# Performance work log

Measured on AMD Instinct MI355X. Metric: run time of the kernel, lower is better.

Reference implementation:

```python
import jax, jax.numpy as jnp
import numpy as np

N = 10000          # nodes
E = 80000          # edges
STATE_DIM = 18
HID = 1024
LAYERS = 4


def setup_inputs() -> dict:
    key = jax.random.key(0)
    ks = jax.random.split(key, 16)
    s = 0.02
    x = jax.random.normal(ks[0], (N, STATE_DIM), dtype=jnp.float32)
    edge_index = jax.random.randint(ks[1], (2, E), 0, N, dtype=jnp.int32)
    # frozen inverse-phase embedding projection (no bias)
    proj_w = jax.random.normal(ks[2], (STATE_DIM, HID), dtype=jnp.float32) * s
    # per-layer message MLP: Linear(2*HID -> HID) -> ReLU -> Linear(HID -> HID)
    W1 = jax.random.normal(ks[3], (LAYERS, 2 * HID, HID), dtype=jnp.float32) * s
    b1 = jnp.zeros((LAYERS, HID), dtype=jnp.float32)
    W2 = jax.random.normal(ks[4], (LAYERS, HID, HID), dtype=jnp.float32) * s
    b2 = jnp.zeros((LAYERS, HID), dtype=jnp.float32)
    # ghost head: Linear(HID->256) -> ReLU -> Linear(256->1) -> Sigmoid
    gw1 = jax.random.normal(ks[5], (HID, 256), dtype=jnp.float32) * s
    gb1 = jnp.zeros((256,), dtype=jnp.float32)
    gw2 = jax.random.normal(ks[6], (256, 1), dtype=jnp.float32) * s
    gb2 = jnp.zeros((1,), dtype=jnp.float32)
    # state head: Linear(HID -> STATE_DIM)
    sw = jax.random.normal(ks[7], (HID, STATE_DIM), dtype=jnp.float32) * s
    sb = jnp.zeros((STATE_DIM,), dtype=jnp.float32)
    return {"x": x, "edge_index": edge_index, "proj_w": proj_w,
            "W1": W1, "b1": b1, "W2": W2, "b2": b2,
            "gw1": gw1, "gb1": gb1, "gw2": gw2, "gb2": gb2,
            "sw": sw, "sb": sb}


def reference(x, edge_index, proj_w, W1, b1, W2, b2, gw1, gb1, gw2, gb2, sw, sb):
    src = edge_index[0]  # j (source)
    dst = edge_index[1]  # i (target), aggr='add' scatters into i
    # InversePhaseEmbedding: sin(h)*cos(h)
    p = x @ proj_w                      # [N, HID]
    h = jnp.sin(p) * jnp.cos(p)
    for l in range(LAYERS):
        x_i = h[dst]                    # [E, HID] gather target feats
        x_j = h[src]                    # [E, HID] gather source feats
        msg = jnp.concatenate([x_i, x_j - x_i], axis=-1)  # [E, 2*HID]
        m = jax.nn.relu(msg @ W1[l] + b1[l]) @ W2[l] + b2[l]  # [E, HID]
        h = jax.ops.segment_sum(m, dst, num_segments=N)       # scatter-add
        h = jax.nn.relu(h)
    ghost_score = jax.nn.sigmoid(jax.nn.relu(h @ gw1 + gb1) @ gw2 + gb2)  # [N,1]
    stable_state = h @ sw + sb                                            # [N,18]
    return ghost_score, stable_state, h
```

## Files before the change

kernel.cpp:

```cpp
#include <hip/hip_runtime.h>
#include <hip/hip_bf16.h>
#include <math.h>

#define NN 10000
#define EE 80000
#define SDIM 18
#define HID 1024
#define NLAYERS 4
#define GHID 256

typedef __bf16 bf16;
typedef __bf16 bf16x8 __attribute__((ext_vector_type(8)));
typedef __bf16 bf16x4 __attribute__((ext_vector_type(4)));
typedef float f32x4 __attribute__((ext_vector_type(4)));

#define AS1C(p) ((const __attribute__((address_space(1))) void*)(p))
#define AS3(p)  ((__attribute__((address_space(3))) void*)(p))

__global__ void count_kernel(const int* __restrict__ ei, int* __restrict__ cnt) {
    int e = blockIdx.x * 256 + threadIdx.x;
    if (e < EE) atomicAdd(&cnt[ei[EE + e]], 1);
}

__global__ __launch_bounds__(256) void scan_kernel(const int* __restrict__ cnt,
                                                   int* __restrict__ offs,
                                                   int* __restrict__ cursor,
                                                   float* __restrict__ degF) {
    const int CH = 40;
    __shared__ int partial[256];
    int t = threadIdx.x;
    int base = t * CH;
    int local[CH];
    int sum = 0;
#pragma unroll
    for (int i = 0; i < CH; ++i) {
        int idx = base + i;
        int v = (idx < NN) ? cnt[idx] : 0;
        local[i] = sum;
        sum += v;
    }
    partial[t] = sum;
    __syncthreads();
    for (int off = 1; off < 256; off <<= 1) {
        int v = (t >= off) ? partial[t - off] : 0;
        __syncthreads();
        partial[t] += v;
        __syncthreads();
    }
    int excl = (t == 0) ? 0 : partial[t - 1];
#pragma unroll
    for (int i = 0; i < CH; ++i) {
        int idx = base + i;
        if (idx < NN) {
            int o = excl + local[i];
            offs[idx] = o;
            cursor[idx] = o;
            degF[idx] = (float)cnt[idx];
        }
    }
    if (t == 255) offs[NN] = partial[255];
}

__global__ void scatter_kernel(const int* __restrict__ ei, int* __restrict__ cursor,
                               int* __restrict__ esrc) {
    int e = blockIdx.x * 256 + threadIdx.x;
    if (e < EE) {
        int dst = ei[EE + e];
        int pos = atomicAdd(&cursor[dst], 1);
        esrc[pos] = ei[e];
    }
}

__global__ __launch_bounds__(256) void prep_kernel(const float* __restrict__ W1,
                                                   const float* __restrict__ W2,
                                                   const float* __restrict__ gw1,
                                                   const float* __restrict__ sw,
                                                   const float* __restrict__ b1,
                                                   bf16* __restrict__ WT,
                                                   bf16* __restrict__ W2t,
                                                   bf16* __restrict__ gw1t,
                                                   bf16* __restrict__ swt,
                                                   float* __restrict__ cb,
                                                   int* __restrict__ cnt) {
    __shared__ float td[32][33];
    __shared__ float tb[32][33];
    const size_t H2 = (size_t)HID * HID;
    int b = blockIdx.x;
    int tx = threadIdx.x & 31, ty = threadIdx.x >> 5;

    if (b < 4096) {
        int l = b >> 10, r = b & 1023;
        int bx = (r & 31) * 32, by = (r >> 5) * 32;
        const float* s = W1 + (size_t)l * 2 * H2;
        bf16* d = WT + (size_t)l * 2 * H2;
#pragma unroll
        for (int r4 = 0; r4 < 4; ++r4) {
            int row = by + ty + r4 * 8;
            float vt = s[(size_t)row * HID + bx + tx];
            float vb = s[H2 + (size_t)row * HID + bx + tx];
            td[ty + r4 * 8][tx] = vt - vb;
            tb[ty + r4 * 8][tx] = vb;
        }
        __syncthreads();
#pragma unroll
        for (int r4 = 0; r4 < 4; ++r4) {
            int orow = bx + ty + r4 * 8;
            d[(size_t)orow * HID + by + tx] = (bf16)td[tx][ty + r4 * 8];
            d[(size_t)(HID + orow) * HID + by + tx] = (bf16)tb[tx][ty + r4 * 8];
        }
    } else if (b < 8192) {
        int sub = b - 4096;
        int l = sub >> 10, r = sub & 1023;
        int bx = (r & 31) * 32, by = (r >> 5) * 32;
        const float* s = W2 + (size_t)l * H2;
        bf16* d = W2t + (size_t)l * H2;
#pragma unroll
        for (int r4 = 0; r4 < 4; ++r4) {
            int row = by + ty + r4 * 8;
            td[ty + r4 * 8][tx] = s[(size_t)row * HID + bx + tx];
        }
        __syncthreads();
#pragma unroll
        for (int r4 = 0; r4 < 4; ++r4) {
            int orow = bx + ty + r4 * 8;
            d[(size_t)orow * HID + by + tx] = (bf16)td[tx][ty + r4 * 8];
        }
    } else if (b < 8448) {
        int sub = b - 8192;
        int bx = (sub & 7) * 32, by = (sub >> 3) * 32;
#pragma unroll
        for (int r4 = 0; r4 < 4; ++r4) {
            int row = by + ty + r4 * 8;
            td[ty + r4 * 8][tx] = gw1[(size_t)row * GHID + bx + tx];
        }
        __syncthreads();
#pragma unroll
        for (int r4 = 0; r4 < 4; ++r4) {
            int orow = bx + ty + r4 * 8;
            gw1t[(size_t)orow * HID + by + tx] = (bf16)td[tx][ty + r4 * 8];
        }
    } else if (b < 8576) {
        int i = (b - 8448) * 256 + threadIdx.x;
        int n = i >> 10, k = i & 1023;
        swt[i] = (bf16)(n < SDIM ? sw[k * SDIM + n] : 0.f);
    } else if (b < 8608) {
        int i = (b - 8576) * 256 + threadIdx.x;
        int l = i >> 11, c = i & 2047;
        cb[i] = (c < HID) ? b1[l * HID + c] : 0.f;
    } else {
        int i = (b - 8608) * 256 + threadIdx.x;
        if (i < NN) cnt[i] = 0;
    }
}

__global__ __launch_bounds__(256) void proj_kernel(const float* __restrict__ x,
                                                   const float* __restrict__ pw,
                                                   bf16* __restrict__ hb) {
    int row = blockIdx.y;
    int col = blockIdx.x * 256 + threadIdx.x;
    __shared__ float xr[SDIM];
    if (threadIdx.x < SDIM) xr[threadIdx.x] = x[row * SDIM + threadIdx.x];
    __syncthreads();
    float acc = 0.f;
#pragma unroll
    for (int k = 0; k < SDIM; ++k) acc += xr[k] * pw[k * HID + col];
    hb[(size_t)row * HID + col] = (bf16)(sinf(acc) * cosf(acc));
}

template <int RELU, int HAS_BIAS, int HAS_RS, int WF32, int WB16>
__global__ __launch_bounds__(256, 3) void mgemm3_kernel(const bf16* __restrict__ A,
                                                        const bf16* __restrict__ Bt,
                                                        float* __restrict__ C,
                                                        bf16* __restrict__ Cb,
                                                        const float* __restrict__ bias,
                                                        const float* __restrict__ rowscale,
                                                        int M, int N, int K) {
    __shared__ bf16 lds[24576];
    const int tid = threadIdx.x;
    const int wave = tid >> 6, lane = tid & 63;
    const int wm = wave >> 1, wn = wave & 1;
    const int quad = lane >> 4, r15 = lane & 15;

    const int num_n = gridDim.x, num_m = gridDim.y;
    int bid = blockIdx.x + blockIdx.y * num_n;
    const int GROUP = 8;
    int width = GROUP * num_n;
    int group = bid / width;
    int rem = bid - group * width;
    int rows_ing = num_m - group * GROUP;
    rows_ing = rows_ing < GROUP ? rows_ing : GROUP;
    int by = group * GROUP + rem % rows_ing;
    int bx = rem / rows_ing;
    const int m0 = by * 128, n0 = bx * 128;

    const int strow = tid >> 2;
    const int segsw = ((tid & 3) ^ ((tid >> 3) & 3)) * 8;
    int ar0 = m0 + strow;       ar0 = ar0 < M ? ar0 : M - 1;
    int ar1 = m0 + 64 + strow;  ar1 = ar1 < M ? ar1 : M - 1;
    const bf16* ga0 = A + (size_t)ar0 * K + segsw;
    const bf16* ga1 = A + (size_t)ar1 * K + segsw;
    const bf16* gb0 = Bt + (size_t)(n0 + strow) * K + segsw;
    const bf16* gb1 = Bt + (size_t)(n0 + 64 + strow) * K + segsw;
    const int ldst = (tid & ~63) * 8;

    int aoff[4], boff[4];
#pragma unroll
    for (int i = 0; i < 4; ++i) {
        int rA = wm * 64 + i * 16 + r15;
        aoff[i] = 12288 + rA * 32 + (quad ^ ((rA >> 1) & 3)) * 8;
        int rB = wn * 64 + i * 16 + r15;
        boff[i] = rB * 32 + (quad ^ ((rB >> 1) & 3)) * 8;
    }

    f32x4 acc[4][4] = {};

#define STAGE3(bs, kt)                                                                                   \
    do {                                                                                                 \
        const int ko_ = (kt) << 5;                                                                       \
        __builtin_amdgcn_global_load_lds(AS1C(ga0 + ko_), AS3(&lds[12288 + (bs)*4096 + ldst]), 16, 0, 0); \
        __builtin_amdgcn_global_load_lds(AS1C(ga1 + ko_), AS3(&lds[12288 + (bs)*4096 + 2048 + ldst]), 16, 0, 0); \
        __builtin_amdgcn_global_load_lds(AS1C(gb0 + ko_), AS3(&lds[(bs)*4096 + ldst]), 16, 0, 0);        \
        __builtin_amdgcn_global_load_lds(AS1C(gb1 + ko_), AS3(&lds[(bs)*4096 + 2048 + ldst]), 16, 0, 0); \
    } while (0)

    STAGE3(0, 0);
    STAGE3(1, 1);
    asm volatile("s_waitcnt vmcnt(4)");
    __builtin_amdgcn_s_barrier();

    const int NT = K >> 5;
    int t = 0;

#define TILE3(bi, bs)                                                                          \
    do {                                                                                       \
        int kt = (t + 2 < NT) ? (t + 2) : (t - 1);  \
        bf16x8 aF[4], bF[4];                                                                   \
        _Pragma("unroll") for (int i = 0; i < 4; ++i)                                          \
            aF[i] = *(const bf16x8*)(&lds[(bi)*4096 + aoff[i]]);                               \
        _Pragma("unroll") for (int j = 0; j < 4; ++j)                                          \
            bF[j] = *(const bf16x8*)(&lds[(bi)*4096 + boff[j]]);                               \
        STAGE3(bs, kt);                                                                        \
        asm volatile("s_waitcnt lgkmcnt(0)");                                                  \
        __builtin_amdgcn_s_setprio(1);                                                         \
        _Pragma("unroll") for (int i = 0; i < 4; ++i)                                          \
            _Pragma("unroll") for (int j = 0; j < 4; ++j)                                      \
                acc[i][j] = __builtin_amdgcn_mfma_f32_16x16x32_bf16(aF[i], bF[j], acc[i][j], 0, 0, 0); \
        __builtin_amdgcn_s_setprio(0);                                                         \
        asm volatile("s_waitcnt vmcnt(4)");          \
        __builtin_amdgcn_s_barrier();                                                          \
        ++t;                                                                                   \
    } while (0)

    while (t + 3 <= NT) { TILE3(0, 2); TILE3(1, 0); TILE3(2, 1); }
    if (t < NT) TILE3(0, 2);
    if (t < NT) TILE3(1, 0);
#undef TILE3
#undef STAGE3

#pragma unroll
    for (int i = 0; i < 4; ++i) {
#pragma unroll
        for (int r = 0; r < 4; ++r) {
            int grow = m0 + wm * 64 + i * 16 + quad * 4 + r;
            if (grow >= M) continue;
            float rs = HAS_RS ? rowscale[grow] : 1.f;
#pragma unroll
            for (int j = 0; j < 4; ++j) {
                int gcol = n0 + wn * 64 + j * 16 + r15;
                float v = acc[i][j][r];
                if (HAS_BIAS) v += rs * bias[gcol];
                if (RELU) v = fmaxf(v, 0.f);
                if (WF32) C[(size_t)grow * N + gcol] = v;
                if (WB16) Cb[(size_t)grow * N + gcol] = (bf16)v;
            }
        }
    }
}

__global__ __launch_bounds__(256) void gather_kernel(const int* __restrict__ offs,
                                                     const int* __restrict__ esrc,
                                                     const bf16* __restrict__ CB,
                                                     bf16* __restrict__ Sb) {
    int half = threadIdx.x >> 7;
    int t = threadIdx.x & 127;
    int node = blockIdx.x * 2 + half;
    int c = t * 8;
    int k0 = offs[node], k1 = offs[node + 1];
    bf16x8 cv = *(const bf16x8*)(CB + (size_t)node * 2048 + c);
    float cf[8], a[8];
#pragma unroll
    for (int i = 0; i < 8; ++i) { cf[i] = (float)cv[i]; a[i] = 0.f; }
    for (int k = k0; k < k1; ++k) {
        int s = esrc[k];
        bf16x8 bv = *(const bf16x8*)(CB + (size_t)s * 2048 + 1024 + c);
#pragma unroll
        for (int i = 0; i < 8; ++i) a[i] += fmaxf(cf[i] + (float)bv[i], 0.f);
    }
    bf16x8 o;
#pragma unroll
    for (int i = 0; i < 8; ++i) o[i] = (bf16)a[i];
    *(bf16x8*)(Sb + (size_t)node * HID + c) = o;
}

__global__ __launch_bounds__(64) void stable_mfma_kernel(const bf16* __restrict__ hb,
                                                         const bf16* __restrict__ swt,
                                                         const float* __restrict__ sb,
                                                         float* __restrict__ out) {
    int m0 = blockIdx.x * 16;
    int lane = threadIdx.x;
    int quad = lane >> 4, r15 = lane & 15;
    f32x4 acc0 = {}, acc1 = {};
    const bf16* arow = hb + (size_t)(m0 + r15) * HID + quad * 8;
    const bf16* b0 = swt + (size_t)r15 * HID + quad * 8;
    const bf16* b1p = swt + (size_t)(16 + r15) * HID + quad * 8;
    for (int k0 = 0; k0 < HID; k0 += 32) {
        bf16x8 af = *(const bf16x8*)(arow + k0);
        bf16x8 bf0 = *(const bf16x8*)(b0 + k0);
        bf16x8 bf1 = *(const bf16x8*)(b1p + k0);
        acc0 = __builtin_amdgcn_mfma_f32_16x16x32_bf16(af, bf0, acc0, 0, 0, 0);
        acc1 = __builtin_amdgcn_mfma_f32_16x16x32_bf16(af, bf1, acc1, 0, 0, 0);
    }
#pragma unroll
    for (int r = 0; r < 4; ++r) {
        int grow = m0 + quad * 4 + r;
        out[(size_t)grow * SDIM + r15] = acc0[r] + sb[r15];
        if (r15 < 2) out[(size_t)grow * SDIM + 16 + r15] = acc1[r] + sb[16 + r15];
    }
}

__global__ __launch_bounds__(256) void ghost_kernel(const float* __restrict__ g1,
                                                    const float* __restrict__ gw2,
                                                    const float* __restrict__ gb2,
                                                    float* __restrict__ out) {
    int w = threadIdx.x >> 6, lane = threadIdx.x & 63;
    int row = blockIdx.x * 4 + w;
    const float4 gv = *(const float4*)(g1 + (size_t)row * GHID + lane * 4);
    const float4 wv = *(const float4*)(gw2 + lane * 4);
    float v = gv.x * wv.x + gv.y * wv.y + gv.z * wv.z + gv.w * wv.w;
#pragma unroll
    for (int o = 32; o > 0; o >>= 1) v += __shfl_down(v, o, 64);
    if (lane == 0) out[row] = 1.f / (1.f + expf(-(v + gb2[0])));
}

extern "C" void kernel_launch(void* const* d_in, const int* in_sizes, int n_in,
                              void* d_out, int out_size, void* d_ws, size_t ws_size,
                              hipStream_t stream) {
    const float* x   = (const float*)d_in[0];
    const int*   ei  = (const int*)d_in[1];
    const float* pw  = (const float*)d_in[2];
    const float* W1  = (const float*)d_in[3];
    const float* b1  = (const float*)d_in[4];
    const float* W2  = (const float*)d_in[5];
    const float* b2  = (const float*)d_in[6];
    const float* gw1 = (const float*)d_in[7];
    const float* gb1 = (const float*)d_in[8];
    const float* gw2 = (const float*)d_in[9];
    const float* gb2 = (const float*)d_in[10];
    const float* sw  = (const float*)d_in[11];
    const float* sb  = (const float*)d_in[12];

    float* out    = (float*)d_out;
    float* ghost  = out;
    float* stable = out + NN;
    float* h      = out + NN + NN * SDIM;

    const size_t H2 = (size_t)HID * HID;
    float* ws   = (float*)d_ws;
    float* g1   = ws;
    float* degF = g1 + (size_t)NN * GHID;
    float* cb   = degF + NN;
    bf16* hb    = (bf16*)(cb + 4 * 2048);
    bf16* Sb    = hb + (size_t)NN * HID;
    bf16* CB    = Sb + (size_t)NN * HID;
    bf16* WT    = CB + (size_t)NN * 2048;
    bf16* W2t   = WT + 8 * H2;
    bf16* gw1t  = W2t + 4 * H2;
    bf16* swt   = gw1t + (size_t)GHID * HID;
    int*  cnt    = (int*)(swt + 32 * 1024);
    int*  offs   = cnt + NN;
    int*  cursor = offs + NN + 1;
    int*  esrc   = cursor + NN;

    prep_kernel<<<dim3(8648), 256, 0, stream>>>(W1, W2, gw1, sw, b1, WT, W2t, gw1t, swt, cb, cnt);

    count_kernel<<<dim3((EE + 255) / 256), 256, 0, stream>>>(ei, cnt);
    scan_kernel<<<dim3(1), 256, 0, stream>>>(cnt, offs, cursor, degF);
    scatter_kernel<<<dim3((EE + 255) / 256), 256, 0, stream>>>(ei, cursor, esrc);

    proj_kernel<<<dim3(HID / 256, NN), 256, 0, stream>>>(x, pw, hb);

    dim3 gcbg(2048 / 128, (NN + 127) / 128);
    dim3 gw2grid(HID / 128, (NN + 127) / 128);
    for (int l = 0; l < NLAYERS; ++l) {
        mgemm3_kernel<0, 1, 0, 0, 1><<<gcbg, 256, 0, stream>>>(
            hb, WT + (size_t)l * 2 * H2, nullptr, CB, cb + l * 2048, nullptr, NN, 2048, HID);
        gather_kernel<<<dim3(NN / 2), 256, 0, stream>>>(offs, esrc, CB, Sb);
        if (l < NLAYERS - 1)
            mgemm3_kernel<1, 1, 1, 0, 1><<<gw2grid, 256, 0, stream>>>(
                Sb, W2t + (size_t)l * H2, nullptr, hb, b2 + (size_t)l * HID, degF, NN, HID, HID);
        else
            mgemm3_kernel<1, 1, 1, 1, 1><<<gw2grid, 256, 0, stream>>>(
                Sb, W2t + (size_t)l * H2, h, hb, b2 + (size_t)l * HID, degF, NN, HID, HID);
    }

    mgemm3_kernel<1, 1, 0, 1, 0><<<dim3(GHID / 128, (NN + 127) / 128), 256, 0, stream>>>(
        hb, gw1t, g1, nullptr, gb1, nullptr, NN, GHID, HID);
    ghost_kernel<<<dim3(NN / 4), 256, 0, stream>>>(g1, gw2, gb2, ghost);
    stable_mfma_kernel<<<dim3(NN / 16), 64, 0, stream>>>(hb, swt, sb, stable);
}
```

Measured before the change: 716.1 us.

## Use 256x128 eight-wave tiles for the message-MLP first-layer GEMM

```diff
diff --git a/kernel.cpp b/kernel.cpp
--- a/kernel.cpp
+++ b/kernel.cpp
@@ -168,13 +168,121 @@
 }
 
 template <int RELU, int HAS_BIAS, int HAS_RS, int WF32, int WB16>
-__global__ __launch_bounds__(256, 3) void mgemm3_kernel(const bf16* __restrict__ A,
+__global__ __launch_bounds__(512, 4) void mgemm3_kernel(const bf16* __restrict__ A,
                                                         const bf16* __restrict__ Bt,
                                                         float* __restrict__ C,
                                                         bf16* __restrict__ Cb,
                                                         const float* __restrict__ bias,
                                                         const float* __restrict__ rowscale,
                                                         int M, int N, int K) {
+    __shared__ bf16 lds[36864];
+    const int tid = threadIdx.x;
+    const int wave = tid >> 6, lane = tid & 63;
+    const int wm = wave >> 1, wn = wave & 1;
+    const int quad = lane >> 4, r15 = lane & 15;
+
+    const int num_n = gridDim.x, num_m = gridDim.y;
+    int bid = blockIdx.x + blockIdx.y * num_n;
+    const int GROUP = 8;
+    int width = GROUP * num_n;
+    int group = bid / width;
+    int rem = bid - group * width;
+    int rows_ing = num_m - group * GROUP;
+    rows_ing = rows_ing < GROUP ? rows_ing : GROUP;
+    int by = group * GROUP + rem % rows_ing;
+    int bx = rem / rows_ing;
+    const int m0 = by * 256, n0 = bx * 128;
+
+    const int strow = tid >> 2;
+    const int segsw = ((tid & 3) ^ ((tid >> 3) & 3)) * 8;
+    int ar0 = m0 + strow;        ar0 = ar0 < M ? ar0 : M - 1;
+    int ar1 = m0 + 128 + strow;  ar1 = ar1 < M ? ar1 : M - 1;
+    const bf16* ga0 = A + (size_t)ar0 * K + segsw;
+    const bf16* ga1 = A + (size_t)ar1 * K + segsw;
+    const bf16* gb  = Bt + (size_t)(n0 + strow) * K + segsw;
+    const int ldst = (tid & ~63) * 8;
+
+    int aoff[4], boff[4];
+#pragma unroll
+    for (int i = 0; i < 4; ++i) {
+        int rA = wm * 64 + i * 16 + r15;
+        aoff[i] = 12288 + rA * 32 + (quad ^ ((rA >> 1) & 3)) * 8;
+        int rB = wn * 64 + i * 16 + r15;
+        boff[i] = rB * 32 + (quad ^ ((rB >> 1) & 3)) * 8;
+    }
+
+    f32x4 acc[4][4] = {};
+
+#define STAGE3(bs, kt)                                                                                \
+    do {                                                                                              \
+        const int ko_ = (kt) << 5;                                                                    \
+        __builtin_amdgcn_global_load_lds(AS1C(ga0 + ko_), AS3(&lds[12288 + (bs)*8192 + ldst]), 16, 0, 0); \
+        __builtin_amdgcn_global_load_lds(AS1C(ga1 + ko_), AS3(&lds[12288 + (bs)*8192 + 4096 + ldst]), 16, 0, 0); \
+        __builtin_amdgcn_global_load_lds(AS1C(gb + ko_), AS3(&lds[(bs)*4096 + ldst]), 16, 0, 0);      \
+    } while (0)
+
+    STAGE3(0, 0);
+    STAGE3(1, 1);
+    asm volatile("s_waitcnt vmcnt(3)");
+    __builtin_amdgcn_s_barrier();
+
+    const int NT = K >> 5;
+    int t = 0;
+
+#define TILE3(bi, bs)                                                                          \
+    do {                                                                                       \
+        int kt = (t + 2 < NT) ? (t + 2) : (t - 1);                                             \
+        bf16x8 aF[4], bF[4];                                                                   \
+        _Pragma("unroll") for (int i = 0; i < 4; ++i)                                          \
+            aF[i] = *(const bf16x8*)(&lds[(bi)*8192 + aoff[i]]);                               \
+        _Pragma("unroll") for (int j = 0; j < 4; ++j)                                          \
+            bF[j] = *(const bf16x8*)(&lds[(bi)*4096 + boff[j]]);                               \
+        STAGE3(bs, kt);                                                                        \
+        asm volatile("s_waitcnt lgkmcnt(0)");                                                  \
+        __builtin_amdgcn_s_setprio(1);                                                         \
+        _Pragma("unroll") for (int i = 0; i < 4; ++i)                                          \
+            _Pragma("unroll") for (int j = 0; j < 4; ++j)                                      \
+                acc[i][j] = __builtin_amdgcn_mfma_f32_16x16x32_bf16(aF[i], bF[j], acc[i][j], 0, 0, 0); \
+        __builtin_amdgcn_s_setprio(0);                                                         \
+        asm volatile("s_waitcnt vmcnt(3)");                                                    \
+        __builtin_amdgcn_s_barrier();                                                          \
+        ++t;                                                                                   \
+    } while (0)
+
+    while (t + 3 <= NT) { TILE3(0, 2); TILE3(1, 0); TILE3(2, 1); }
+    if (t < NT) TILE3(0, 2);
+    if (t < NT) TILE3(1, 0);
+#undef TILE3
+#undef STAGE3
+
+#pragma unroll
+    for (int i = 0; i < 4; ++i) {
+#pragma unroll
+        for (int r = 0; r < 4; ++r) {
+            int grow = m0 + wm * 64 + i * 16 + quad * 4 + r;
+            if (grow >= M) continue;
+            float rs = HAS_RS ? rowscale[grow] : 1.f;
+#pragma unroll
+            for (int j = 0; j < 4; ++j) {
+                int gcol = n0 + wn * 64 + j * 16 + r15;
+                float v = acc[i][j][r];
+                if (HAS_BIAS) v += rs * bias[gcol];
+                if (RELU) v = fmaxf(v, 0.f);
+                if (WF32) C[(size_t)grow * N + gcol] = v;
+                if (WB16) Cb[(size_t)grow * N + gcol] = (bf16)v;
+            }
+        }
+    }
+}
+
+template <int RELU, int HAS_BIAS, int HAS_RS, int WF32, int WB16>
+__global__ __launch_bounds__(256, 3) void mgemm3h_kernel(const bf16* __restrict__ A,
+                                                         const bf16* __restrict__ Bt,
+                                                         float* __restrict__ C,
+                                                         bf16* __restrict__ Cb,
+                                                         const float* __restrict__ bias,
+                                                         const float* __restrict__ rowscale,
+                                                         int M, int N, int K) {
     __shared__ bf16 lds[24576];
     const int tid = threadIdx.x;
     const int wave = tid >> 6, lane = tid & 63;
@@ -214,7 +322,7 @@
 
     f32x4 acc[4][4] = {};
 
-#define STAGE3(bs, kt)                                                                                   \
+#define STAGE3H(bs, kt)                                                                                  \
     do {                                                                                                 \
         const int ko_ = (kt) << 5;                                                                       \
         __builtin_amdgcn_global_load_lds(AS1C(ga0 + ko_), AS3(&lds[12288 + (bs)*4096 + ldst]), 16, 0, 0); \
@@ -223,39 +331,39 @@
         __builtin_amdgcn_global_load_lds(AS1C(gb1 + ko_), AS3(&lds[(bs)*4096 + 2048 + ldst]), 16, 0, 0); \
     } while (0)
 
-    STAGE3(0, 0);
-    STAGE3(1, 1);
+    STAGE3H(0, 0);
+    STAGE3H(1, 1);
     asm volatile("s_waitcnt vmcnt(4)");
     __builtin_amdgcn_s_barrier();
 
     const int NT = K >> 5;
     int t = 0;
 
-#define TILE3(bi, bs)                                                                          \
+#define TILE3H(bi, bs)                                                                         \
     do {                                                                                       \
-        int kt = (t + 2 < NT) ? (t + 2) : (t - 1);  \
+        int kt = (t + 2 < NT) ? (t + 2) : (t - 1);                                             \
         bf16x8 aF[4], bF[4];                                                                   \
         _Pragma("unroll") for (int i = 0; i < 4; ++i)                                          \
             aF[i] = *(const bf16x8*)(&lds[(bi)*4096 + aoff[i]]);                               \
         _Pragma("unroll") for (int j = 0; j < 4; ++j)                                          \
             bF[j] = *(const bf16x8*)(&lds[(bi)*4096 + boff[j]]);                               \
-        STAGE3(bs, kt);                                                                        \
+        STAGE3H(bs, kt);                                                                       \
         asm volatile("s_waitcnt lgkmcnt(0)");                                                  \
         __builtin_amdgcn_s_setprio(1);                                                         \
         _Pragma("unroll") for (int i = 0; i < 4; ++i)                                          \
             _Pragma("unroll") for (int j = 0; j < 4; ++j)                                      \
                 acc[i][j] = __builtin_amdgcn_mfma_f32_16x16x32_bf16(aF[i], bF[j], acc[i][j], 0, 0, 0); \
         __builtin_amdgcn_s_setprio(0);                                                         \
-        asm volatile("s_waitcnt vmcnt(4)");          \
+        asm volatile("s_waitcnt vmcnt(4)");                                                    \
         __builtin_amdgcn_s_barrier();                                                          \
         ++t;                                                                                   \
     } while (0)
 
-    while (t + 3 <= NT) { TILE3(0, 2); TILE3(1, 0); TILE3(2, 1); }
-    if (t < NT) TILE3(0, 2);
-    if (t < NT) TILE3(1, 0);
-#undef TILE3
-#undef STAGE3
+    while (t + 3 <= NT) { TILE3H(0, 2); TILE3H(1, 0); TILE3H(2, 1); }
+    if (t < NT) TILE3H(0, 2);
+    if (t < NT) TILE3H(1, 0);
+#undef TILE3H
+#undef STAGE3H
 
 #pragma unroll
     for (int i = 0; i < 4; ++i) {
@@ -389,21 +497,21 @@
 
     proj_kernel<<<dim3(HID / 256, NN), 256, 0, stream>>>(x, pw, hb);
 
-    dim3 gcbg(2048 / 128, (NN + 127) / 128);
+    dim3 gcbg(2048 / 128, (NN + 255) / 256);
     dim3 gw2grid(HID / 128, (NN + 127) / 128);
     for (int l = 0; l < NLAYERS; ++l) {
-        mgemm3_kernel<0, 1, 0, 0, 1><<<gcbg, 256, 0, stream>>>(
+        mgemm3_kernel<0, 1, 0, 0, 1><<<gcbg, 512, 0, stream>>>(
             hb, WT + (size_t)l * 2 * H2, nullptr, CB, cb + l * 2048, nullptr, NN, 2048, HID);
         gather_kernel<<<dim3(NN / 2), 256, 0, stream>>>(offs, esrc, CB, Sb);
         if (l < NLAYERS - 1)
-            mgemm3_kernel<1, 1, 1, 0, 1><<<gw2grid, 256, 0, stream>>>(
+            mgemm3h_kernel<1, 1, 1, 0, 1><<<gw2grid, 256, 0, stream>>>(
                 Sb, W2t + (size_t)l * H2, nullptr, hb, b2 + (size_t)l * HID, degF, NN, HID, HID);
         else
-            mgemm3_kernel<1, 1, 1, 1, 1><<<gw2grid, 256, 0, stream>>>(
+            mgemm3h_kernel<1, 1, 1, 1, 1><<<gw2grid, 256, 0, stream>>>(
                 Sb, W2t + (size_t)l * H2, h, hb, b2 + (size_t)l * HID, degF, NN, HID, HID);
     }
 
-    mgemm3_kernel<1, 1, 0, 1, 0><<<dim3(GHID / 128, (NN + 127) / 128), 256, 0, stream>>>(
+    mgemm3h_kernel<1, 1, 0, 1, 0><<<dim3(GHID / 128, (NN + 127) / 128), 256, 0, stream>>>(
         hb, gw1t, g1, nullptr, gb1, nullptr, NN, GHID, HID);
     ghost_kernel<<<dim3(NN / 4), 256, 0, stream>>>(g1, gw2, gb2, ghost);
     stable_mfma_kernel<<<dim3(NN / 16), 64, 0, stream>>>(hb, swt, sb, stable);
```

New measurement: 710.5 us. About the same (-0.8%).
